# Kernel optimization log

Measured on AMD Instinct MI355X. Metric: run time of the kernel, lower is better.

Reference implementation:

```python
import jax, jax.numpy as jnp
import numpy as np

TEMPERATURE = 0.07
LOSS_CL_WEIGHT = 1.0
EPS = 1e-12  # F.normalize default eps


def setup_inputs() -> dict:
    key = jax.random.key(0)
    k1, k2 = jax.random.split(key)
    N, S, D = 64, 64, 256
    return {
        "proj_z1": jax.random.normal(k1, (N, S, D), dtype=jnp.float32),
        "proj_z2": jax.random.normal(k2, (N, S, D), dtype=jnp.float32),
    }


def _clean_normalize(x, NS, D):
    # flatten -> replace nan/inf with 0 -> L2 normalize rows
    x = x.reshape(NS, D)
    x = jnp.where(jnp.isfinite(x), x, jnp.zeros((), x.dtype))
    norm = jnp.linalg.norm(x, axis=1, keepdims=True)
    return x / jnp.maximum(norm, EPS)


def reference(proj_z1, proj_z2):
    N, S, D = proj_z1.shape
    NS = N * S
    M = 2 * NS
    f1 = _clean_normalize(proj_z1, NS, D)
    f2 = _clean_normalize(proj_z2, NS, D)
    features = jnp.concatenate([f1, f2], axis=0)          # (M, D)
    sim = features @ features.T                            # (M, M)

    idx = jnp.arange(M)
    # positive pair: row i <-> row (i + NS) mod M (eye blocks in label_matrix)
    positives = sim[idx, (idx + NS) % M] / TEMPERATURE     # (M,)
    # CE denominator = all off-diagonal entries (positives + negatives)
    scores = sim / TEMPERATURE
    scores = jnp.where(idx[:, None] == idx[None, :], -jnp.inf, scores)
    lse = jax.nn.logsumexp(scores, axis=1)                 # (M,)
    loss = jnp.mean(lse - positives)
    return LOSS_CL_WEIGHT * loss
```

## Files before the change

kernel.cpp:

```cpp
#include <hip/hip_runtime.h>
#include <stdint.h>

#define NS_ 4096
#define M_  8192
#define D_  256
#define TEMP 0.07f
#define EXP_SCALE 20.61707212818536f
#define LN2 0.6931471805599453f

typedef short bf16x8 __attribute__((ext_vector_type(8)));
typedef float f32x4  __attribute__((ext_vector_type(4)));
typedef unsigned short ushortx4 __attribute__((ext_vector_type(4)));

static __device__ inline unsigned short f2bf(float x) {
    unsigned u = __float_as_uint(x);
    u += 0x7fffu + ((u >> 16) & 1u);
    return (unsigned short)(u >> 16);
}

static __device__ inline float cleanf(float v) {
    return __builtin_isfinite(v) ? v : 0.0f;
}

#define LDS_LOAD16(gp, lp) \
    __builtin_amdgcn_global_load_lds((const __attribute__((address_space(1))) uint32_t*)(gp), \
                                     (__attribute__((address_space(3))) uint32_t*)(lp), 16, 0, 0)

__global__ __launch_bounds__(256) void knorm(const float* __restrict__ z1,
                                             const float* __restrict__ z2,
                                             short* __restrict__ F,
                                             float* __restrict__ pos,
                                             float* __restrict__ denom,
                                             int* __restrict__ cnt,
                                             float* __restrict__ out) {
    const int wave = threadIdx.x >> 6;
    const int t    = threadIdx.x & 63;
    const int i    = blockIdx.x * 4 + wave;
    const float4* p1 = (const float4*)(z1 + (size_t)i * D_);
    const float4* p2 = (const float4*)(z2 + (size_t)i * D_);
    float4 a = p1[t], b = p2[t];
    a.x = cleanf(a.x); a.y = cleanf(a.y); a.z = cleanf(a.z); a.w = cleanf(a.w);
    b.x = cleanf(b.x); b.y = cleanf(b.y); b.z = cleanf(b.z); b.w = cleanf(b.w);

    float s1 = a.x*a.x + a.y*a.y + a.z*a.z + a.w*a.w;
    float s2 = b.x*b.x + b.y*b.y + b.z*b.z + b.w*b.w;
    float dp = a.x*b.x + a.y*b.y + a.z*b.z + a.w*b.w;
    #pragma unroll
    for (int m = 1; m < 64; m <<= 1) {
        s1 += __shfl_xor(s1, m);
        s2 += __shfl_xor(s2, m);
        dp += __shfl_xor(dp, m);
    }
    const float inv1 = 1.0f / fmaxf(sqrtf(s1), 1e-12f);
    const float inv2 = 1.0f / fmaxf(sqrtf(s2), 1e-12f);

    ushortx4 o1, o2;
    o1.x = f2bf(a.x * inv1); o1.y = f2bf(a.y * inv1); o1.z = f2bf(a.z * inv1); o1.w = f2bf(a.w * inv1);
    o2.x = f2bf(b.x * inv2); o2.y = f2bf(b.y * inv2); o2.z = f2bf(b.z * inv2); o2.w = f2bf(b.w * inv2);
    ((ushortx4*)(F + (size_t)i * D_))[t]          = o1;
    ((ushortx4*)(F + (size_t)(i + NS_) * D_))[t]  = o2;

    if (t == 0) pos[i] = dp * inv1 * inv2;
    if (t < 2)  denom[i * 2 + t] = 0.0f;
    if (i == 0 && t < 32) cnt[t] = 0;
    if (i == 0 && t == 0) out[0] = 0.0f;
}

__global__ __launch_bounds__(512, 1) void kgemm(const short* __restrict__ F,
                                                float* __restrict__ denom,
                                                int* __restrict__ cnt,
                                                const float* __restrict__ pos,
                                                float* __restrict__ out) {
    __shared__ short Bl[3][64 * 256];
    __shared__ int lastflag;
    __shared__ float red[8];

    const int rtile = blockIdx.x >> 3;
    const int cq    = blockIdx.x & 7;
    const int R0 = rtile * 256;
    const int C0 = cq * 1024;

    const int tid  = threadIdx.x;
    const int lane = tid & 63;
    const int wave = tid >> 6;
    const int c16  = lane & 15;
    const int quad = lane >> 4;
    const int swz  = c16 & 7;

    int goff[4];
    #pragma unroll
    for (int r2 = 0; r2 < 4; ++r2) {
        int g   = tid + r2 * 512;
        int row = g >> 5;
        int kg  = (g & 31) ^ (row & 7);
        goff[r2] = row * D_ + kg * 8;
    }

    const short* baseA = F + (size_t)R0 * D_;
    const short* baseB = F + (size_t)C0 * D_;

    short* const bufs0 = &Bl[0][0];
    short* const bufs1 = &Bl[1][0];
    short* const bufs2 = &Bl[2][0];

    bf16x8 afrag[2][8];
    const int mych = wave >> 1;
    const int lrb  = (wave & 1) * 32;

    {
        #pragma unroll
        for (int r2 = 0; r2 < 4; ++r2)
            LDS_LOAD16(baseA + goff[r2], bufs0 + (tid + r2 * 512) * 8);
    }
    #pragma unroll
    for (int ch = 0; ch < 4; ++ch) {
        const short* nxt = (ch < 3) ? (baseA + (size_t)(ch + 1) * 64 * D_) : baseB;
        short* dst = (ch == 0) ? bufs1 : (ch == 1) ? bufs2 : (ch == 2) ? bufs0 : bufs1;
        #pragma unroll
        for (int r2 = 0; r2 < 4; ++r2)
            LDS_LOAD16(nxt + goff[r2], dst + (tid + r2 * 512) * 8);
        asm volatile("s_waitcnt vmcnt(4)" ::: "memory");
        __builtin_amdgcn_s_barrier();
        if (mych == ch) {
            const short* bp = (ch == 0) ? bufs0 : (ch == 1) ? bufs1 : (ch == 2) ? bufs2 : bufs0;
            #pragma unroll
            for (int st = 0; st < 2; ++st) {
                const int row = lrb + st * 16 + c16;
                #pragma unroll
                for (int ks = 0; ks < 8; ++ks)
                    afrag[st][ks] = *(const bf16x8*)(bp + row * 256 +
                                                     (((ks * 4 + quad) ^ swz) * 8));
            }
        }
        asm volatile("s_waitcnt lgkmcnt(0)" ::: "memory");
        __builtin_amdgcn_s_barrier();
    }
    {
        const short* gb = baseB + (size_t)64 * D_;
        #pragma unroll
        for (int r2 = 0; r2 < 4; ++r2)
            LDS_LOAD16(gb + goff[r2], bufs2 + (tid + r2 * 512) * 8);
    }

    float accexp[2][4];
    #pragma unroll
    for (int st = 0; st < 2; ++st)
        #pragma unroll
        for (int r = 0; r < 4; ++r) accexp[st][r] = 0.0f;

    short* pr = bufs1;
    short* pn = bufs2;
    short* ps = bufs0;

    for (int t = 0; t < 16; ++t) {
        if (t < 15) { asm volatile("s_waitcnt vmcnt(4)" ::: "memory"); }
        else        { asm volatile("s_waitcnt vmcnt(0)" ::: "memory"); }
        __builtin_amdgcn_s_barrier();
        const short* gb2 = baseB + (size_t)(t + 2) * 64 * D_;

        #pragma unroll
        for (int sub = 0; sub < 4; ++sub) {
            const int tc = sub * 16 + c16;
            bf16x8 bfrag[8];
            #pragma unroll
            for (int ks = 0; ks < 8; ++ks)
                bfrag[ks] = *(const bf16x8*)(pr + tc * 256 +
                                             (((ks * 4 + quad) ^ swz) * 8));
            if (t < 14)
                LDS_LOAD16(gb2 + goff[sub], ps + (tid + sub * 512) * 8);

            f32x4 acc0 = (f32x4){0.f, 0.f, 0.f, 0.f};
            f32x4 acc1 = (f32x4){0.f, 0.f, 0.f, 0.f};
            __builtin_amdgcn_s_setprio(1);
            #pragma unroll
            for (int ks = 0; ks < 8; ++ks) {
                acc0 = __builtin_amdgcn_mfma_f32_16x16x32_bf16(afrag[0][ks], bfrag[ks], acc0, 0, 0, 0);
                acc1 = __builtin_amdgcn_mfma_f32_16x16x32_bf16(afrag[1][ks], bfrag[ks], acc1, 0, 0, 0);
            }
            __builtin_amdgcn_s_setprio(0);

            const int colbase = C0 + t * 64 + sub * 16;
            #pragma unroll
            for (int st = 0; st < 2; ++st) {
                const f32x4 acc = st ? acc1 : acc0;
                const int rowbase = R0 + wave * 32 + st * 16;
                if (colbase != rowbase) {
                    #pragma unroll
                    for (int r = 0; r < 4; ++r)
                        accexp[st][r] += __builtin_amdgcn_exp2f(acc[r] * EXP_SCALE);
                } else {
                    #pragma unroll
                    for (int r = 0; r < 4; ++r) {
                        float e = __builtin_amdgcn_exp2f(acc[r] * EXP_SCALE);
                        if (c16 == quad * 4 + r) e = 0.0f;
                        accexp[st][r] += e;
                    }
                }
            }
        }
        short* tmp = pr; pr = pn; pn = ps; ps = tmp;
    }

    #pragma unroll
    for (int st = 0; st < 2; ++st)
        #pragma unroll
        for (int r = 0; r < 4; ++r) {
            float v = accexp[st][r];
            v += __shfl_xor(v, 1);
            v += __shfl_xor(v, 2);
            v += __shfl_xor(v, 4);
            v += __shfl_xor(v, 8);
            if (c16 == 0)
                atomicAdd(&denom[R0 + wave * 32 + st * 16 + quad * 4 + r], v);
        }

    __syncthreads();
    if (tid == 0) {
        __threadfence();
        lastflag = (atomicAdd(&cnt[rtile], 1) == 7);
    }
    __syncthreads();
    if (lastflag) {
        __threadfence();
        float p = 0.0f;
        if (tid < 256) {
            float v = atomicAdd(&denom[R0 + tid], 0.0f);
            p = __builtin_amdgcn_logf(v) * (LN2 / (float)M_);
        }
        #pragma unroll
        for (int m = 1; m < 64; m <<= 1) p += __shfl_xor(p, m);
        if (lane == 0) red[wave] = p;
        __syncthreads();
        if (tid == 0) atomicAdd(out, red[0] + red[1] + red[2] + red[3] +
                                     red[4] + red[5] + red[6] + red[7]);
        if (rtile == 0) {
            __syncthreads();
            float sp = 0.0f;
            for (int i = tid; i < NS_; i += 512) sp += pos[i];
            #pragma unroll
            for (int m = 1; m < 64; m <<= 1) sp += __shfl_xor(sp, m);
            if (lane == 0) red[wave] = sp;
            __syncthreads();
            if (tid == 0)
                atomicAdd(out, (red[0] + red[1] + red[2] + red[3] +
                                red[4] + red[5] + red[6] + red[7]) *
                               (-2.0f / (TEMP * (float)M_)));
        }
    }
}

extern "C" void kernel_launch(void* const* d_in, const int* in_sizes, int n_in,
                              void* d_out, int out_size, void* d_ws, size_t ws_size,
                              hipStream_t stream) {
    const float* z1 = (const float*)d_in[0];
    const float* z2 = (const float*)d_in[1];

    short* F     = (short*)d_ws;
    float* denom = (float*)((char*)d_ws + (size_t)M_ * D_ * 2);
    int*   cnt   = (int*)(denom + M_);
    float* pos   = (float*)(cnt + 32);
    float* out   = (float*)d_out;

    knorm<<<NS_ / 4, 256, 0, stream>>>(z1, z2, F, pos, denom, cnt, out);
    kgemm<<<256, 512, 0, stream>>>(F, denom, cnt, pos, out);
}
```

Baseline: 111.4 us.

## Drop triple-buffered LDS pipeline for single buffer with higher occupancy and more blocks

Replaces the three-stage LDS ring buffer and its async-load pipelining with a single 32KB buffer guarded by plain __syncthreads, and raises launch bounds to allow 4 blocks per CU. The grid doubles to 512 blocks by halving each block's column range, and the A-fragment row mapping is remapped accordingly. The intent is to hide memory latency through multiple resident blocks instead of explicit in-block prefetch, at the cost of serialized load/compute within each block, a tighter register budget, and removal of the MFMA priority hints.

```diff
diff --git a/kernel.cpp b/kernel.cpp
--- a/kernel.cpp
+++ b/kernel.cpp
@@ -66,19 +66,19 @@
     if (i == 0 && t == 0) out[0] = 0.0f;
 }
 
-__global__ __launch_bounds__(512, 1) void kgemm(const short* __restrict__ F,
+__global__ __launch_bounds__(512, 4) void kgemm(const short* __restrict__ F,
                                                 float* __restrict__ denom,
                                                 int* __restrict__ cnt,
                                                 const float* __restrict__ pos,
                                                 float* __restrict__ out) {
-    __shared__ short Bl[3][64 * 256];
+    __shared__ short Bl[64 * 256];
     __shared__ int lastflag;
     __shared__ float red[8];
 
-    const int rtile = blockIdx.x >> 3;
-    const int cq    = blockIdx.x & 7;
+    const int rtile = blockIdx.x >> 4;
+    const int cq    = blockIdx.x & 15;
     const int R0 = rtile * 256;
-    const int C0 = cq * 1024;
+    const int C0 = cq * 512;
 
     const int tid  = threadIdx.x;
     const int lane = tid & 63;
@@ -90,73 +90,44 @@
     int goff[4];
     #pragma unroll
     for (int r2 = 0; r2 < 4; ++r2) {
-        int g   = tid + r2 * 512;
-        int row = g >> 5;
-        int kg  = (g & 31) ^ (row & 7);
+        int c    = tid + r2 * 512;
+        int row  = c >> 5;
+        int kg   = (c & 31) ^ (row & 7);
         goff[r2] = row * D_ + kg * 8;
     }
 
-    const short* baseA = F + (size_t)R0 * D_;
-    const short* baseB = F + (size_t)C0 * D_;
-
-    short* const bufs0 = &Bl[0][0];
-    short* const bufs1 = &Bl[1][0];
-    short* const bufs2 = &Bl[2][0];
-
     bf16x8 afrag[2][8];
-    const int mych = wave >> 1;
-    const int lrb  = (wave & 1) * 32;
-
-    {
+    #pragma unroll
+    for (int ch = 0; ch < 4; ++ch) {
+        __syncthreads();
+        const short* ga = F + (size_t)(R0 + ch * 64) * D_;
         #pragma unroll
         for (int r2 = 0; r2 < 4; ++r2)
-            LDS_LOAD16(baseA + goff[r2], bufs0 + (tid + r2 * 512) * 8);
-    }
-    #pragma unroll
-    for (int ch = 0; ch < 4; ++ch) {
-        const short* nxt = (ch < 3) ? (baseA + (size_t)(ch + 1) * 64 * D_) : baseB;
-        short* dst = (ch == 0) ? bufs1 : (ch == 1) ? bufs2 : (ch == 2) ? bufs0 : bufs1;
+            LDS_LOAD16(ga + goff[r2], Bl + (tid + r2 * 512) * 8);
+        __syncthreads();
+        const int st = ch >> 1;
+        if ((wave >> 2) == (ch & 1)) {
+            const int lrow = (wave & 3) * 16 + c16;
+            #pragma unroll
+            for (int ks = 0; ks < 8; ++ks)
+                afrag[st][ks] = *(const bf16x8*)(Bl + lrow * 256 +
+                                                 (((ks * 4 + quad) ^ swz) * 8));
+        }
+    }
+
+    float accexp[2][4];
+    #pragma unroll
+    for (int st = 0; st < 2; ++st)
+        #pragma unroll
+        for (int r = 0; r < 4; ++r) accexp[st][r] = 0.0f;
+
+    for (int it = 0; it < 8; ++it) {
+        __syncthreads();
+        const short* gb = F + (size_t)(C0 + it * 64) * D_;
         #pragma unroll
         for (int r2 = 0; r2 < 4; ++r2)
-            LDS_LOAD16(nxt + goff[r2], dst + (tid + r2 * 512) * 8);
-        asm volatile("s_waitcnt vmcnt(4)" ::: "memory");
-        __builtin_amdgcn_s_barrier();
-        if (mych == ch) {
-            const short* bp = (ch == 0) ? bufs0 : (ch == 1) ? bufs1 : (ch == 2) ? bufs2 : bufs0;
-            #pragma unroll
-            for (int st = 0; st < 2; ++st) {
-                const int row = lrb + st * 16 + c16;
-                #pragma unroll
-                for (int ks = 0; ks < 8; ++ks)
-                    afrag[st][ks] = *(const bf16x8*)(bp + row * 256 +
-                                                     (((ks * 4 + quad) ^ swz) * 8));
-            }
-        }
-        asm volatile("s_waitcnt lgkmcnt(0)" ::: "memory");
-        __builtin_amdgcn_s_barrier();
-    }
-    {
-        const short* gb = baseB + (size_t)64 * D_;
-        #pragma unroll
-        for (int r2 = 0; r2 < 4; ++r2)
-            LDS_LOAD16(gb + goff[r2], bufs2 + (tid + r2 * 512) * 8);
-    }
-
-    float accexp[2][4];
-    #pragma unroll
-    for (int st = 0; st < 2; ++st)
-        #pragma unroll
-        for (int r = 0; r < 4; ++r) accexp[st][r] = 0.0f;
-
-    short* pr = bufs1;
-    short* pn = bufs2;
-    short* ps = bufs0;
-
-    for (int t = 0; t < 16; ++t) {
-        if (t < 15) { asm volatile("s_waitcnt vmcnt(4)" ::: "memory"); }
-        else        { asm volatile("s_waitcnt vmcnt(0)" ::: "memory"); }
-        __builtin_amdgcn_s_barrier();
-        const short* gb2 = baseB + (size_t)(t + 2) * 64 * D_;
+            LDS_LOAD16(gb + goff[r2], Bl + (tid + r2 * 512) * 8);
+        __syncthreads();
 
         #pragma unroll
         for (int sub = 0; sub < 4; ++sub) {
@@ -164,26 +135,21 @@
             bf16x8 bfrag[8];
             #pragma unroll
             for (int ks = 0; ks < 8; ++ks)
-                bfrag[ks] = *(const bf16x8*)(pr + tc * 256 +
+                bfrag[ks] = *(const bf16x8*)(Bl + tc * 256 +
                                              (((ks * 4 + quad) ^ swz) * 8));
-            if (t < 14)
-                LDS_LOAD16(gb2 + goff[sub], ps + (tid + sub * 512) * 8);
-
             f32x4 acc0 = (f32x4){0.f, 0.f, 0.f, 0.f};
             f32x4 acc1 = (f32x4){0.f, 0.f, 0.f, 0.f};
-            __builtin_amdgcn_s_setprio(1);
             #pragma unroll
             for (int ks = 0; ks < 8; ++ks) {
                 acc0 = __builtin_amdgcn_mfma_f32_16x16x32_bf16(afrag[0][ks], bfrag[ks], acc0, 0, 0, 0);
                 acc1 = __builtin_amdgcn_mfma_f32_16x16x32_bf16(afrag[1][ks], bfrag[ks], acc1, 0, 0, 0);
             }
-            __builtin_amdgcn_s_setprio(0);
-
-            const int colbase = C0 + t * 64 + sub * 16;
+
+            const int colbase = C0 + it * 64 + sub * 16;
             #pragma unroll
             for (int st = 0; st < 2; ++st) {
                 const f32x4 acc = st ? acc1 : acc0;
-                const int rowbase = R0 + wave * 32 + st * 16;
+                const int rowbase = R0 + st * 128 + wave * 16;
                 if (colbase != rowbase) {
                     #pragma unroll
                     for (int r = 0; r < 4; ++r)
@@ -198,7 +164,6 @@
                 }
             }
         }
-        short* tmp = pr; pr = pn; pn = ps; ps = tmp;
     }
 
     #pragma unroll
@@ -211,13 +176,13 @@
             v += __shfl_xor(v, 4);
             v += __shfl_xor(v, 8);
             if (c16 == 0)
-                atomicAdd(&denom[R0 + wave * 32 + st * 16 + quad * 4 + r], v);
+                atomicAdd(&denom[R0 + st * 128 + wave * 16 + quad * 4 + r], v);
         }
 
     __syncthreads();
     if (tid == 0) {
         __threadfence();
-        lastflag = (atomicAdd(&cnt[rtile], 1) == 7);
+        lastflag = (atomicAdd(&cnt[rtile], 1) == 15);
     }
     __syncthreads();
     if (lastflag) {
@@ -262,5 +227,5 @@
     float* out   = (float*)d_out;
 
     knorm<<<NS_ / 4, 256, 0, stream>>>(z1, z2, F, pos, denom, cnt, out);
-    kgemm<<<256, 512, 0, stream>>>(F, denom, cnt, pos, out);
-}
+    kgemm<<<512, 512, 0, stream>>>(F, denom, cnt, pos, out);
+}
```

After: 146.6 us. 31.5% more time.
